# Kernel optimization log

Measured on AMD Instinct MI355X. Metric: run time of the kernel, lower is better.

Reference implementation:

```python
import jax, jax.numpy as jnp
import numpy as np

N = 8192
D = 256
DENSITY = 0.02  # ~164 neighbors per node


def setup_inputs() -> dict:
    key = jax.random.key(0)
    k1, k2, k3, k4 = jax.random.split(key, 4)
    inputs = jax.random.normal(k1, (N, D), dtype=jnp.float32)
    vals = jax.random.uniform(k2, (N, N), dtype=jnp.float32, minval=0.1, maxval=1.0)
    mask = jax.random.uniform(k3, (N, N), dtype=jnp.float32) < DENSITY
    adj = jnp.where(mask, vals, 0.0)
    H_v = 0.1 * jax.random.normal(k4, (D, 1), dtype=jnp.float32)
    return {"inputs": inputs, "adj": adj, "H_v": H_v}


def reference(inputs, adj, H_v):
    # scores[j] = inputs[j] . H_v  -> sparse values v_ij = adj_ij * scores[j]
    scores = jnp.squeeze(inputs @ H_v, -1)            # [N]
    mask = adj != 0.0                                  # nonzero pattern of SparseTensor
    logits = adj * scores[None, :]                     # [N, N]
    neg = jnp.asarray(jnp.finfo(logits.dtype).min, logits.dtype)
    logits = jnp.where(mask, logits, neg)
    # sparse softmax: normalize only over nonzero entries per row
    m = jnp.max(logits, axis=1, keepdims=True)
    e = jnp.where(mask, jnp.exp(logits - m), 0.0)
    s = jnp.sum(e, axis=1, keepdims=True)
    weights = e / jnp.where(s > 0, s, 1.0)             # empty rows -> all-zero weights
    # sparse_tensor_dense_matmul(weights, inputs)
    return weights @ inputs                            # [N, D]
```

## Files before the change

### kernel.cpp

```cpp
#include <hip/hip_runtime.h>

#define NN 8192
#define DD 256
#define RT 32
#define KC 128
#define KS 4
#define KRANGE (NN / KS)
#define NCH (KRANGE / KC)

typedef float v4f __attribute__((ext_vector_type(4)));
typedef short short8 __attribute__((ext_vector_type(8)));
typedef float f32x4 __attribute__((ext_vector_type(4)));
typedef unsigned short u16x4 __attribute__((ext_vector_type(4)));
typedef unsigned short u16x8 __attribute__((ext_vector_type(8)));

__device__ __forceinline__ unsigned short f2bf_rne(float x) {
    unsigned u = __float_as_uint(x);
    u += 0x7fffu + ((u >> 16) & 1u);
    return (unsigned short)(u >> 16);
}
__device__ __forceinline__ float bf_to_f(unsigned short b) {
    return __uint_as_float((unsigned)b << 16);
}

__global__ __launch_bounds__(256) void scores_kernel(const float* __restrict__ inputs,
                                                     const float* __restrict__ Hv,
                                                     float* __restrict__ scores) {
    int wave = threadIdx.x >> 6;
    int lane = threadIdx.x & 63;
    int row  = blockIdx.x * 4 + wave;
    if (row >= NN) return;
    float4 v = ((const float4*)(inputs + (size_t)row * DD))[lane];
    float4 h = ((const float4*)Hv)[lane];
    float s = v.x * h.x + v.y * h.y + v.z * h.z + v.w * h.w;
    #pragma unroll
    for (int off = 32; off > 0; off >>= 1) s += __shfl_down(s, off, 64);
    if (lane == 0) scores[row] = s;
}

#define XP 258
__global__ __launch_bounds__(256) void xtp_kernel(const float* __restrict__ inputs,
                                                  unsigned short* __restrict__ xtp) {
    __shared__ unsigned short sx[64 * XP];
    const int tid = threadIdx.x;
    const int k0  = blockIdx.x * 64;
    #pragma unroll
    for (int r = 0; r < 16; ++r) {
        int row = r * 4 + (tid >> 6);
        int col = (tid & 63) * 4;
        float4 v = *(const float4*)(inputs + (size_t)(k0 + row) * DD + col);
        u16x4 w;
        w[0] = f2bf_rne(v.x); w[1] = f2bf_rne(v.y); w[2] = f2bf_rne(v.z); w[3] = f2bf_rne(v.w);
        *(u16x4*)&sx[row * XP + col] = w;
    }
    __syncthreads();
    #pragma unroll
    for (int r = 0; r < 8; ++r) {
        int rid  = r * 256 + tid;
        int lane = rid & 63;
        int t    = (rid >> 6) & 15;
        int kcl  = rid >> 10;
        int n    = t * 16 + (lane & 15);
        int kl   = kcl * 32 + (lane >> 4) * 8;
        u16x8 w;
        #pragma unroll
        for (int j = 0; j < 8; ++j) w[j] = sx[(kl + j) * XP + n];
        size_t kcg = (size_t)(k0 >> 5) + kcl;
        *(u16x8*)(xtp + (((size_t)t * 256 + kcg) * 64 + lane) * 8) = w;
    }
}

__global__ __launch_bounds__(512, 4) void spmm_kernel(const float* __restrict__ adj,
                                                      const unsigned short* __restrict__ xtp,
                                                      const float* __restrict__ scores,
                                                      float* __restrict__ pc,
                                                      float* __restrict__ pd) {
    __shared__ unsigned short sE[2][RT * KC];
    __shared__ float sS[KRANGE];

    const int tid  = threadIdx.x;
    const int lane = tid & 63;
    const int wave = tid >> 6;
    const int q    = lane >> 4;
    const int m16  = lane & 15;

    const int ks    = blockIdx.x & (KS - 1);
    const int mb    = blockIdx.x >> 2;
    const int row0  = mb * RT;
    const int kbase = ks * KRANGE;

    ((float4*)sS)[tid] = ((const float4*)(scores + kbase))[tid];

    const int lrow = tid >> 4;
    const int kgb  = tid & 15;
    const int kg   = kgb * 8;
    const float* arow = adj + (size_t)(row0 + lrow) * NN + kbase;

    f32x4 acc[2][2] = {};
    float den = 0.f;

    v4f pa[2][2];
    pa[0][0] = __builtin_nontemporal_load((const v4f*)(arow + kg));
    pa[0][1] = __builtin_nontemporal_load((const v4f*)(arow + kg + 4));
    pa[1][0] = __builtin_nontemporal_load((const v4f*)(arow + KC + kg));
    pa[1][1] = __builtin_nontemporal_load((const v4f*)(arow + KC + kg + 4));

    __syncthreads();

    for (int c = 0; c < NCH; ++c) {
        const int s = c & 1;

        const size_t kcg0 = (size_t)((kbase + c * KC) >> 5);
        short8 bfr[2][4];
        #pragma unroll
        for (int nt = 0; nt < 2; ++nt) {
            const size_t t = (size_t)(wave * 2 + nt);
            #pragma unroll
            for (int kh = 0; kh < 4; ++kh)
                bfr[nt][kh] = *(const short8*)(xtp + ((t * 256 + kcg0 + kh) * 64 + lane) * 8);
        }

        float af[8] = { pa[s][0].x, pa[s][0].y, pa[s][0].z, pa[s][0].w,
                        pa[s][1].x, pa[s][1].y, pa[s][1].z, pa[s][1].w };
        u16x8 ev;
        #pragma unroll
        for (int i = 0; i < 8; ++i) {
            float a = af[i];
            float e = (a != 0.f) ? __expf(a * sS[c * KC + kg + i]) : 0.f;
            unsigned short b = f2bf_rne(e);
            ev[i] = b;
            den += bf_to_f(b);
        }

        if (c + 2 < NCH) {
            pa[s][0] = __builtin_nontemporal_load((const v4f*)(arow + (c + 2) * KC + kg));
            pa[s][1] = __builtin_nontemporal_load((const v4f*)(arow + (c + 2) * KC + kg + 4));
        }

        *(u16x8*)&sE[s][lrow * KC + ((kgb ^ (lrow & 15)) * 8)] = ev;
        __syncthreads();

        const unsigned short* Eb = sE[s];
        #pragma unroll
        for (int kh = 0; kh < 4; ++kh) {
            short8 a0 = *(const short8*)&Eb[m16 * KC + (((kh * 4 + q) ^ m16) * 8)];
            short8 a1 = *(const short8*)&Eb[(16 + m16) * KC + (((kh * 4 + q) ^ m16) * 8)];
            acc[0][0] = __builtin_amdgcn_mfma_f32_16x16x32_bf16(a0, bfr[0][kh], acc[0][0], 0, 0, 0);
            acc[0][1] = __builtin_amdgcn_mfma_f32_16x16x32_bf16(a0, bfr[1][kh], acc[0][1], 0, 0, 0);
            acc[1][0] = __builtin_amdgcn_mfma_f32_16x16x32_bf16(a1, bfr[0][kh], acc[1][0], 0, 0, 0);
            acc[1][1] = __builtin_amdgcn_mfma_f32_16x16x32_bf16(a1, bfr[1][kh], acc[1][1], 0, 0, 0);
        }
    }

    #pragma unroll
    for (int d = 1; d < 16; d <<= 1) den += __shfl_xor(den, d, 64);
    if ((tid & 15) == 0) pd[(size_t)ks * NN + row0 + lrow] = den;

    float* pcb = pc + ((size_t)ks * NN + row0) * DD;
    #pragma unroll
    for (int mt = 0; mt < 2; ++mt)
        #pragma unroll
        for (int nt = 0; nt < 2; ++nt)
            #pragma unroll
            for (int r = 0; r < 4; ++r) {
                int rr = mt * 16 + q * 4 + r;
                pcb[(size_t)rr * DD + wave * 32 + nt * 16 + m16] = acc[mt][nt][r];
            }
}

__global__ __launch_bounds__(256) void reduce_kernel(const float* __restrict__ pc,
                                                     const float* __restrict__ pd,
                                                     float* __restrict__ out) {
    const int row = blockIdx.x;
    const int tid = threadIdx.x;
    float d = 0.f, v = 0.f;
    #pragma unroll
    for (int ks = 0; ks < KS; ++ks) {
        d += pd[(size_t)ks * NN + row];
        v += pc[((size_t)ks * NN + row) * DD + tid];
    }
    out[(size_t)row * DD + tid] = (d > 0.f) ? v / d : 0.f;
}

__global__ __launch_bounds__(256) void attn_fallback(const float* __restrict__ adj,
                                                     const float* __restrict__ inputs,
                                                     const float* __restrict__ scores,
                                                     float* __restrict__ out) {
    __shared__ int   s_j[1024];
    __shared__ float s_e[1024];
    __shared__ int   s_cnt;
    const int row = blockIdx.x;
    const int tid = threadIdx.x;
    const float* arow = adj + (size_t)row * NN;
    float acc = 0.f, ssum = 0.f;
    for (int base = 0; base < NN; base += 1024) {
        if (tid == 0) s_cnt = 0;
        __syncthreads();
        float4 a = ((const float4*)(arow + base))[tid];
        int j0 = base + tid * 4;
        if (a.x != 0.f) { int k = atomicAdd(&s_cnt, 1); s_j[k] = j0 + 0; s_e[k] = __expf(a.x * scores[j0 + 0]); }
        if (a.y != 0.f) { int k = atomicAdd(&s_cnt, 1); s_j[k] = j0 + 1; s_e[k] = __expf(a.y * scores[j0 + 1]); }
        if (a.z != 0.f) { int k = atomicAdd(&s_cnt, 1); s_j[k] = j0 + 2; s_e[k] = __expf(a.z * scores[j0 + 2]); }
        if (a.w != 0.f) { int k = atomicAdd(&s_cnt, 1); s_j[k] = j0 + 3; s_e[k] = __expf(a.w * scores[j0 + 3]); }
        __syncthreads();
        int c = s_cnt;
        for (int k = 0; k < c; ++k) {
            float e = s_e[k];
            acc  += e * inputs[(size_t)s_j[k] * DD + tid];
            ssum += e;
        }
        __syncthreads();
    }
    out[(size_t)row * DD + tid] = (ssum > 0.f) ? acc / ssum : 0.f;
}

extern "C" void kernel_launch(void* const* d_in, const int* in_sizes, int n_in,
                              void* d_out, int out_size, void* d_ws, size_t ws_size,
                              hipStream_t stream) {
    const float* inputs = (const float*)d_in[0];
    const float* adj    = (const float*)d_in[1];
    const float* Hv     = (const float*)d_in[2];
    float* out = (float*)d_out;

    char* ws = (char*)d_ws;
    float*          scores = (float*)ws;
    unsigned short* xtp    = (unsigned short*)(ws + 32768);
    float*          pd     = (float*)(ws + 32768 + (size_t)NN * DD * 2);
    float*          pc     = (float*)(ws + 32768 + (size_t)NN * DD * 2 + KS * NN * 4);

    const size_t need = 32768 + (size_t)NN * DD * 2 + (size_t)KS * NN * 4
                      + (size_t)KS * NN * DD * 4;

    scores_kernel<<<NN / 4, 256, 0, stream>>>(inputs, Hv, scores);
    if (ws_size >= need) {
        xtp_kernel<<<NN / 64, 256, 0, stream>>>(inputs, xtp);
        spmm_kernel<<<(NN / RT) * KS, 512, 0, stream>>>(adj, xtp, scores, pc, pd);
        reduce_kernel<<<NN, 256, 0, stream>>>(pc, pd, out);
    } else {
        attn_fallback<<<NN, 256, 0, stream>>>(adj, inputs, scores, out);
    }
}
```

Before: 411.5 us.

## Double row tile to 64 so each B fragment load feeds more MFMAs

Raises the row tile from 32 to 64 rows per block. Each thread now converts two adjacency rows per chunk, and each wave issues MFMAs over four M-tiles. This halves how often the bf16 transposed inputs are reloaded per output row. The prefetch of adjacency changes from a two-chunk-ahead ring to a one-chunk-ahead register copy. The cost is more registers and LDS per block, half as many blocks, and a shallower prefetch of the adjacency stream.

```diff
diff --git a/kernel.cpp b/kernel.cpp
--- a/kernel.cpp
+++ b/kernel.cpp
@@ -2,7 +2,7 @@
 
 #define NN 8192
 #define DD 256
-#define RT 32
+#define RT 64
 #define KC 128
 #define KS 4
 #define KRANGE (NN / KS)
@@ -94,21 +94,29 @@
     const int lrow = tid >> 4;
     const int kgb  = tid & 15;
     const int kg   = kgb * 8;
-    const float* arow = adj + (size_t)(row0 + lrow) * NN + kbase;
-
-    f32x4 acc[2][2] = {};
-    float den = 0.f;
-
-    v4f pa[2][2];
-    pa[0][0] = __builtin_nontemporal_load((const v4f*)(arow + kg));
-    pa[0][1] = __builtin_nontemporal_load((const v4f*)(arow + kg + 4));
-    pa[1][0] = __builtin_nontemporal_load((const v4f*)(arow + KC + kg));
-    pa[1][1] = __builtin_nontemporal_load((const v4f*)(arow + KC + kg + 4));
+    const float* ar0 = adj + (size_t)(row0 + lrow) * NN + kbase;
+    const float* ar1 = ar0 + (size_t)32 * NN;
+
+    f32x4 acc[4][2] = {};
+    float den0 = 0.f, den1 = 0.f;
+
+    v4f a[2][2];
+    a[0][0] = __builtin_nontemporal_load((const v4f*)(ar0 + kg));
+    a[0][1] = __builtin_nontemporal_load((const v4f*)(ar0 + kg + 4));
+    a[1][0] = __builtin_nontemporal_load((const v4f*)(ar1 + kg));
+    a[1][1] = __builtin_nontemporal_load((const v4f*)(ar1 + kg + 4));
 
     __syncthreads();
 
     for (int c = 0; c < NCH; ++c) {
         const int s = c & 1;
+        const int cn = (c + 1 < NCH ? c + 1 : c) * KC;
+
+        v4f na[2][2];
+        na[0][0] = __builtin_nontemporal_load((const v4f*)(ar0 + cn + kg));
+        na[0][1] = __builtin_nontemporal_load((const v4f*)(ar0 + cn + kg + 4));
+        na[1][0] = __builtin_nontemporal_load((const v4f*)(ar1 + cn + kg));
+        na[1][1] = __builtin_nontemporal_load((const v4f*)(ar1 + cn + kg + 4));
 
         const size_t kcg0 = (size_t)((kbase + c * KC) >> 5);
         short8 bfr[2][4];
@@ -120,45 +128,56 @@
                 bfr[nt][kh] = *(const short8*)(xtp + ((t * 256 + kcg0 + kh) * 64 + lane) * 8);
         }
 
-        float af[8] = { pa[s][0].x, pa[s][0].y, pa[s][0].z, pa[s][0].w,
-                        pa[s][1].x, pa[s][1].y, pa[s][1].z, pa[s][1].w };
-        u16x8 ev;
-        #pragma unroll
-        for (int i = 0; i < 8; ++i) {
-            float a = af[i];
-            float e = (a != 0.f) ? __expf(a * sS[c * KC + kg + i]) : 0.f;
-            unsigned short b = f2bf_rne(e);
-            ev[i] = b;
-            den += bf_to_f(b);
-        }
-
-        if (c + 2 < NCH) {
-            pa[s][0] = __builtin_nontemporal_load((const v4f*)(arow + (c + 2) * KC + kg));
-            pa[s][1] = __builtin_nontemporal_load((const v4f*)(arow + (c + 2) * KC + kg + 4));
-        }
-
-        *(u16x8*)&sE[s][lrow * KC + ((kgb ^ (lrow & 15)) * 8)] = ev;
+        #pragma unroll
+        for (int h = 0; h < 2; ++h) {
+            float af[8] = { a[h][0].x, a[h][0].y, a[h][0].z, a[h][0].w,
+                            a[h][1].x, a[h][1].y, a[h][1].z, a[h][1].w };
+            u16x8 ev;
+            float dl = 0.f;
+            #pragma unroll
+            for (int i = 0; i < 8; ++i) {
+                float v = af[i];
+                float e = (v != 0.f) ? __expf(v * sS[c * KC + kg + i]) : 0.f;
+                unsigned short b = f2bf_rne(e);
+                ev[i] = b;
+                dl += bf_to_f(b);
+            }
+            if (h) den1 += dl; else den0 += dl;
+            *(u16x8*)&sE[s][(lrow + 32 * h) * KC + ((kgb ^ (lrow & 15)) * 8)] = ev;
+        }
         __syncthreads();
 
         const unsigned short* Eb = sE[s];
         #pragma unroll
         for (int kh = 0; kh < 4; ++kh) {
-            short8 a0 = *(const short8*)&Eb[m16 * KC + (((kh * 4 + q) ^ m16) * 8)];
-            short8 a1 = *(const short8*)&Eb[(16 + m16) * KC + (((kh * 4 + q) ^ m16) * 8)];
-            acc[0][0] = __builtin_amdgcn_mfma_f32_16x16x32_bf16(a0, bfr[0][kh], acc[0][0], 0, 0, 0);
-            acc[0][1] = __builtin_amdgcn_mfma_f32_16x16x32_bf16(a0, bfr[1][kh], acc[0][1], 0, 0, 0);
-            acc[1][0] = __builtin_amdgcn_mfma_f32_16x16x32_bf16(a1, bfr[0][kh], acc[1][0], 0, 0, 0);
-            acc[1][1] = __builtin_amdgcn_mfma_f32_16x16x32_bf16(a1, bfr[1][kh], acc[1][1], 0, 0, 0);
-        }
-    }
-
-    #pragma unroll
-    for (int d = 1; d < 16; d <<= 1) den += __shfl_xor(den, d, 64);
-    if ((tid & 15) == 0) pd[(size_t)ks * NN + row0 + lrow] = den;
+            short8 A[4];
+            #pragma unroll
+            for (int mt = 0; mt < 4; ++mt)
+                A[mt] = *(const short8*)&Eb[(mt * 16 + m16) * KC + (((kh * 4 + q) ^ m16) * 8)];
+            #pragma unroll
+            for (int mt = 0; mt < 4; ++mt) {
+                acc[mt][0] = __builtin_amdgcn_mfma_f32_16x16x32_bf16(A[mt], bfr[0][kh], acc[mt][0], 0, 0, 0);
+                acc[mt][1] = __builtin_amdgcn_mfma_f32_16x16x32_bf16(A[mt], bfr[1][kh], acc[mt][1], 0, 0, 0);
+            }
+        }
+
+        a[0][0] = na[0][0]; a[0][1] = na[0][1];
+        a[1][0] = na[1][0]; a[1][1] = na[1][1];
+    }
+
+    #pragma unroll
+    for (int d = 1; d < 16; d <<= 1) {
+        den0 += __shfl_xor(den0, d, 64);
+        den1 += __shfl_xor(den1, d, 64);
+    }
+    if ((tid & 15) == 0) {
+        pd[(size_t)ks * NN + row0 + lrow]      = den0;
+        pd[(size_t)ks * NN + row0 + lrow + 32] = den1;
+    }
 
     float* pcb = pc + ((size_t)ks * NN + row0) * DD;
     #pragma unroll
-    for (int mt = 0; mt < 2; ++mt)
+    for (int mt = 0; mt < 4; ++mt)
         #pragma unroll
         for (int nt = 0; nt < 2; ++nt)
             #pragma unroll
```

After: 409.5 us. Within noise of the previous version (-0.5%).
